# Performance work log

Hardware: AMD Instinct MI355X
Metric: run time of the kernel (lower is better)

Reference implementation:

```python
import jax, jax.numpy as jnp
import numpy as np

NEG_SLOPE = 0.2  # PyG GATConv default negative_slope


def _glorot(key, shape):
    fan = shape[0]
    return jax.random.normal(key, shape, dtype=jnp.float32) / np.sqrt(fan)


def setup_inputs() -> dict:
    key = jax.random.key(0)
    ks = jax.random.split(key, 32)
    N, E, C_IN, C_H, C_OUT = 20000, 320000, 128, 640, 2
    inp = {
        "x": jax.random.normal(ks[0], (N, C_IN), dtype=jnp.float32),
        "edge_index": jax.random.randint(ks[1], (2, E), 0, N, dtype=jnp.int64),
    }
    dims = [(C_IN, C_H), (C_H, C_H), (C_H, C_H), (C_H, C_H), (C_H, C_OUT)]
    for i, (ci, co) in enumerate(dims, start=1):
        k = jax.random.split(ks[1 + i], 4)
        inp[f"W{i}"] = _glorot(k[0], (ci, co))
        inp[f"as{i}"] = _glorot(k[1], (co,))
        inp[f"ad{i}"] = _glorot(k[2], (co,))
        inp[f"b{i}"] = jnp.zeros((co,), dtype=jnp.float32)
    return inp


def _gat_conv(h, W, a_src, a_dst, b, src, dst, N):
    # h: [N, Ci] -> hW: [N, Co]
    hW = h @ W
    # per-edge attention logit: LeakyReLU(alpha_src[j] + alpha_dst[i]) for edge j->i
    e = jax.nn.leaky_relu((hW @ a_src)[src] + (hW @ a_dst)[dst], NEG_SLOPE)
    # segment softmax over incoming edges of each dst node (self-loops guarantee nonempty)
    m = jax.ops.segment_max(e, dst, num_segments=N)
    ex = jnp.exp(e - m[dst])
    den = jax.ops.segment_sum(ex, dst, num_segments=N)
    alpha = ex / den[dst]
    # weighted scatter-add of source messages
    out = jax.ops.segment_sum(alpha[:, None] * hW[src], dst, num_segments=N)
    return out + b


def reference(x, edge_index, W1, as1, ad1, b1, W2, as2, ad2, b2, W3, as3, ad3, b3,
              W4, as4, ad4, b4, W5, as5, ad5, b5):
    N = x.shape[0]
    # PyG GATConv default add_self_loops=True
    loops = jnp.arange(N, dtype=edge_index.dtype)
    ei = jnp.concatenate([edge_index, jnp.stack([loops, loops])], axis=1)
    src, dst = ei[0], ei[1]
    h = jax.nn.relu(_gat_conv(x, W1, as1, ad1, b1, src, dst, N))
    h = jax.nn.relu(_gat_conv(h, W2, as2, ad2, b2, src, dst, N))
    h = jax.nn.relu(_gat_conv(h, W3, as3, ad3, b3, src, dst, N))
    h = jax.nn.relu(_gat_conv(h, W4, as4, ad4, b4, src, dst, N))
    # dropout in eval mode = identity
    return _gat_conv(h, W5, as5, ad5, b5, src, dst, N)
```

## Files before the change

kernel.cpp:

```cpp
#include <hip/hip_runtime.h>
#include <math.h>

#define N_NODES 20000
#define MPAD 20096
#define E_EDGES 320000
#define ET (E_EDGES + N_NODES)
#define C_HID 640
#define NEG_SLOPE 0.2f

typedef __attribute__((ext_vector_type(8))) short bf16x8;
typedef __attribute__((ext_vector_type(4))) float f32x4;

__device__ __forceinline__ float leaky(float x) { return x > 0.f ? x : NEG_SLOPE * x; }

__device__ __forceinline__ unsigned short f2bf(float f) {
    unsigned u = __float_as_uint(f);
    unsigned r = (u + 0x7fffu + ((u >> 16) & 1u)) >> 16;
    return (unsigned short)r;
}
__device__ __forceinline__ float bf2f(unsigned short h) {
    return __uint_as_float(((unsigned)h) << 16);
}

__device__ __forceinline__ void gld16(const void* g, void* l) {
    __builtin_amdgcn_global_load_lds((const __attribute__((address_space(1))) unsigned int*)g,
                                     (__attribute__((address_space(3))) unsigned int*)l,
                                     16, 0, 0);
}

__global__ void k_zero(int* p, int n) {
    int i = blockIdx.x * blockDim.x + threadIdx.x;
    if (i < n) p[i] = 0;
}

__global__ void k_zerof(float* p, int n) {
    int i = blockIdx.x * blockDim.x + threadIdx.x;
    if (i < n) p[i] = 0.f;
}

__global__ void k_count(const int* __restrict__ ei, int* __restrict__ counts) {
    int j = blockIdx.x * blockDim.x + threadIdx.x;
    if (j >= ET) return;
    int d = (j < E_EDGES) ? ei[E_EDGES + j] : (j - E_EDGES);
    atomicAdd(&counts[d], 1);
}

__global__ __launch_bounds__(1024) void k_scan(const int* __restrict__ counts,
                                               int* __restrict__ rowptr) {
    __shared__ int part[1024];
    int t = threadIdx.x;
    int base = t * 20;
    int incl[20];
    int s = 0;
#pragma unroll
    for (int k = 0; k < 20; k++) {
        int i = base + k;
        int v = (i < N_NODES) ? counts[i] : 0;
        s += v;
        incl[k] = s;
    }
    part[t] = s;
    __syncthreads();
    for (int off = 1; off < 1024; off <<= 1) {
        int x = (t >= off) ? part[t - off] : 0;
        __syncthreads();
        part[t] += x;
        __syncthreads();
    }
    int prefix = (t == 0) ? 0 : part[t - 1];
    if (t == 0) rowptr[0] = 0;
#pragma unroll
    for (int k = 0; k < 20; k++) {
        int i = base + k;
        if (i < N_NODES) rowptr[i + 1] = prefix + incl[k];
    }
}

__global__ void k_copy(const int* __restrict__ a, int* __restrict__ b, int n) {
    int i = blockIdx.x * blockDim.x + threadIdx.x;
    if (i < n) b[i] = a[i];
}

__global__ void k_fill(const int* __restrict__ ei, int* __restrict__ cursor, int* __restrict__ col) {
    int j = blockIdx.x * blockDim.x + threadIdx.x;
    if (j >= ET) return;
    int s, d;
    if (j < E_EDGES) { s = ei[j]; d = ei[E_EDGES + j]; }
    else { s = d = j - E_EDGES; }
    int pos = atomicAdd(&cursor[d], 1);
    col[pos] = s;
}

__global__ void k_splitx(const float* __restrict__ x, unsigned short* __restrict__ xh,
                         unsigned short* __restrict__ xl) {
    int idx = blockIdx.x * blockDim.x + threadIdx.x;
    if (idx >= MPAD * 128 / 4) return;
    int row = idx >> 5;
    float4 v = make_float4(0.f, 0.f, 0.f, 0.f);
    if (row < N_NODES) v = ((const float4*)x)[idx];
    float a[4] = {v.x, v.y, v.z, v.w};
    unsigned short h[4], l[4];
#pragma unroll
    for (int i = 0; i < 4; i++) {
        h[i] = f2bf(a[i]);
        l[i] = f2bf(a[i] - bf2f(h[i]));
    }
    *(ushort4*)&xh[idx * 4] = make_ushort4(h[0], h[1], h[2], h[3]);
    *(ushort4*)&xl[idx * 4] = make_ushort4(l[0], l[1], l[2], l[3]);
}

__global__ void k_splitW(const float* __restrict__ W, unsigned short* __restrict__ Wth,
                         unsigned short* __restrict__ Wtl, int K) {
    int idx = blockIdx.x * blockDim.x + threadIdx.x;
    if (idx >= K * C_HID) return;
    int k = idx / C_HID, n = idx - k * C_HID;
    float w = W[idx];
    unsigned short h = f2bf(w);
    Wth[n * K + k] = h;
    Wtl[n * K + k] = f2bf(w - bf2f(h));
}

__global__ void k_padzero(unsigned short* __restrict__ ph, unsigned short* __restrict__ pl) {
    int idx = blockIdx.x * blockDim.x + threadIdx.x;
    int total = (MPAD - N_NODES) * C_HID;
    if (idx >= total) return;
    ph[N_NODES * C_HID + idx] = 0;
    pl[N_NODES * C_HID + idx] = 0;
}

__global__ __launch_bounds__(256) void k_mfma_gemm(
    const unsigned short* __restrict__ Ahi, const unsigned short* __restrict__ Alo,
    const unsigned short* __restrict__ Bth, const unsigned short* __restrict__ Btl,
    float* __restrict__ C, int K, int M,
    const float* __restrict__ asrc, const float* __restrict__ adst,
    float* __restrict__ as_, float* __restrict__ ad_) {
    __shared__ unsigned short lds[4 * 128 * 32];
    const int t = threadIdx.x;
    const int lane = t & 63, wv = t >> 6;
    const int wm = wv & 1, wn = wv >> 1;
    const int quad = lane >> 4, cl = lane & 15;
    const int rowBase = blockIdx.x * 128;
    const int colBase = blockIdx.y * 128;
    const int r = t >> 2, c8 = (t & 3) * 8;

    f32x4 acc[4][4];
#pragma unroll
    for (int i = 0; i < 4; i++)
#pragma unroll
        for (int j = 0; j < 4; j++)
            acc[i][j] = (f32x4){0.f, 0.f, 0.f, 0.f};

    for (int k0 = 0; k0 < K; k0 += 32) {
        __syncthreads();
#pragma unroll
        for (int p = 0; p < 2; ++p) {
            int row = p * 64 + r;
            size_t ga = (size_t)(rowBase + row) * K + k0 + c8;
            size_t gb = (size_t)(colBase + row) * K + k0 + c8;
            int lo = row * 32 + c8;
            gld16(Ahi + ga, &lds[lo]);
            gld16(Alo + ga, &lds[4096 + lo]);
            gld16(Bth + gb, &lds[8192 + lo]);
            gld16(Btl + gb, &lds[12288 + lo]);
        }
        __syncthreads();

        bf16x8 ah[4], al[4], bh[4], bl[4];
#pragma unroll
        for (int i = 0; i < 4; ++i) {
            int am = (wm * 64 + i * 16 + cl) * 32 + quad * 8;
            ah[i] = *(const bf16x8*)&lds[am];
            al[i] = *(const bf16x8*)&lds[4096 + am];
            int bn = (wn * 64 + i * 16 + cl) * 32 + quad * 8;
            bh[i] = *(const bf16x8*)&lds[8192 + bn];
            bl[i] = *(const bf16x8*)&lds[12288 + bn];
        }
#pragma unroll
        for (int i = 0; i < 4; ++i)
#pragma unroll
            for (int j = 0; j < 4; ++j) {
                acc[i][j] = __builtin_amdgcn_mfma_f32_16x16x32_bf16(ah[i], bh[j], acc[i][j], 0, 0, 0);
                acc[i][j] = __builtin_amdgcn_mfma_f32_16x16x32_bf16(ah[i], bl[j], acc[i][j], 0, 0, 0);
                acc[i][j] = __builtin_amdgcn_mfma_f32_16x16x32_bf16(al[i], bh[j], acc[i][j], 0, 0, 0);
            }
    }

#pragma unroll
    for (int i = 0; i < 4; ++i)
#pragma unroll
        for (int j = 0; j < 4; ++j) {
            int colC = colBase + wn * 64 + j * 16 + cl;
#pragma unroll
            for (int rr = 0; rr < 4; ++rr) {
                int rowC = rowBase + wm * 64 + i * 16 + quad * 4 + rr;
                if (rowC < M) C[(size_t)rowC * C_HID + colC] = acc[i][j][rr];
            }
        }

    float av[4], dv[4];
#pragma unroll
    for (int j = 0; j < 4; ++j) {
        int cn = colBase + wn * 64 + j * 16 + cl;
        av[j] = asrc[cn];
        dv[j] = adst[cn];
    }
#pragma unroll
    for (int i = 0; i < 4; ++i)
#pragma unroll
        for (int rr = 0; rr < 4; ++rr) {
            float s = 0.f, d = 0.f;
#pragma unroll
            for (int j = 0; j < 4; ++j) {
                float v = acc[i][j][rr];
                s = fmaf(v, av[j], s);
                d = fmaf(v, dv[j], d);
            }
#pragma unroll
            for (int o = 8; o >= 1; o >>= 1) {
                s += __shfl_xor(s, o);
                d += __shfl_xor(d, o);
            }
            int rowC = rowBase + wm * 64 + i * 16 + quad * 4 + rr;
            if (cl == 0 && rowC < M) {
                atomicAdd(&as_[rowC], s);
                atomicAdd(&ad_[rowC], d);
            }
        }
}

__global__ __launch_bounds__(256) void k_gather(const float* __restrict__ hW,
                                                const float* __restrict__ as_,
                                                const float* __restrict__ ad_,
                                                const int* __restrict__ rowptr,
                                                const int* __restrict__ col,
                                                const float* __restrict__ bias,
                                                unsigned short* __restrict__ outh,
                                                unsigned short* __restrict__ outl) {
    int wv = threadIdx.x >> 6, lane = threadIdx.x & 63;
    int node = blockIdx.x * 4 + wv;
    int c = blockIdx.y;
    if (node >= N_NODES) return;
    int start = rowptr[node], end = rowptr[node + 1];
    int deg = end - start;
    const float* base = hW + c * 128 + lane * 2;
    float ax = 0.f, ay = 0.f;
    float adi = ad_[node];

    if (deg <= 64) {
        int col_v = col[start + min(lane, deg - 1)];
        float asv = as_[col_v];
        float logit = (lane < deg) ? leaky(asv + adi) : -1e30f;
        float m = logit;
#pragma unroll
        for (int o = 32; o; o >>= 1) m = fmaxf(m, __shfl_xor(m, o));
        float ex = __expf(logit - m);
        float den = ex;
#pragma unroll
        for (int o = 32; o; o >>= 1) den += __shfl_xor(den, o);
        float alpha_v = ex / den;

        for (int e0 = 0; e0 < deg; e0 += 8) {
            float2 r[8];
            float a[8];
#pragma unroll
            for (int q = 0; q < 8; ++q) {
                int e = e0 + q;
                int ec = min(e, deg - 1);
                int s = __shfl(col_v, ec);
                float ar = __shfl(alpha_v, ec);
                a[q] = (e < deg) ? ar : 0.f;
                r[q] = *(const float2*)(base + (size_t)s * C_HID);
            }
#pragma unroll
            for (int q = 0; q < 8; ++q) {
                ax = fmaf(a[q], r[q].x, ax);
                ay = fmaf(a[q], r[q].y, ay);
            }
        }
    } else {
        float m = -1e30f;
        for (int j = start + lane; j < end; j += 64)
            m = fmaxf(m, leaky(as_[col[j]] + adi));
        for (int o = 32; o; o >>= 1) m = fmaxf(m, __shfl_xor(m, o));
        float den = 0.f;
        for (int j = start + lane; j < end; j += 64)
            den += __expf(leaky(as_[col[j]] + adi) - m);
        for (int o = 32; o; o >>= 1) den += __shfl_xor(den, o);
        float inv = 1.f / den;
        for (int j = start; j < end; ++j) {
            int s = col[j];
            float a = __expf(leaky(as_[s] + adi) - m) * inv;
            float2 r = *(const float2*)(base + (size_t)s * C_HID);
            ax = fmaf(a, r.x, ax);
            ay = fmaf(a, r.y, ay);
        }
    }

    float2 b = *(const float2*)&bias[c * 128 + lane * 2];
    float v0 = fmaxf(ax + b.x, 0.f);
    float v1 = fmaxf(ay + b.y, 0.f);
    unsigned short h0 = f2bf(v0), h1 = f2bf(v1);
    size_t o = (size_t)node * C_HID + c * 128 + lane * 2;
    *(ushort2*)&outh[o] = make_ushort2(h0, h1);
    *(ushort2*)&outl[o] = make_ushort2(f2bf(v0 - bf2f(h0)), f2bf(v1 - bf2f(h1)));
}

__global__ __launch_bounds__(256) void k_gemm2(const unsigned short* __restrict__ hh,
                                               const unsigned short* __restrict__ hl,
                                               const float* __restrict__ W,
                                               const float* __restrict__ asrc,
                                               const float* __restrict__ adst,
                                               float* __restrict__ hW5,
                                               float* __restrict__ as_,
                                               float* __restrict__ ad_) {
    int wave = (blockIdx.x * blockDim.x + threadIdx.x) >> 6;
    int lane = threadIdx.x & 63;
    if (wave >= N_NODES) return;
    const ushort2* rh = (const ushort2*)(hh + (size_t)wave * C_HID);
    const ushort2* rl = (const ushort2*)(hl + (size_t)wave * C_HID);
    float a0 = 0.f, a1 = 0.f;
#pragma unroll
    for (int k2 = lane; k2 < C_HID / 2; k2 += 64) {
        ushort2 h2 = rh[k2];
        ushort2 l2 = rl[k2];
        float v0 = bf2f(h2.x) + bf2f(l2.x);
        float v1 = bf2f(h2.y) + bf2f(l2.y);
        int k = k2 * 2;
        a0 = fmaf(v0, W[k * 2 + 0], a0);
        a1 = fmaf(v0, W[k * 2 + 1], a1);
        a0 = fmaf(v1, W[k * 2 + 2], a0);
        a1 = fmaf(v1, W[k * 2 + 3], a1);
    }
    for (int o = 32; o; o >>= 1) { a0 += __shfl_xor(a0, o); a1 += __shfl_xor(a1, o); }
    if (lane == 0) {
        hW5[wave * 2 + 0] = a0;
        hW5[wave * 2 + 1] = a1;
        as_[wave] = a0 * asrc[0] + a1 * asrc[1];
        ad_[wave] = a0 * adst[0] + a1 * adst[1];
    }
}

__global__ __launch_bounds__(256) void k_agg2(const float* __restrict__ hW5,
                                              const float* __restrict__ as_,
                                              const float* __restrict__ ad_,
                                              const int* __restrict__ rowptr,
                                              const int* __restrict__ col,
                                              const float* __restrict__ bias,
                                              float* __restrict__ out) {
    int wv = threadIdx.x >> 6, lane = threadIdx.x & 63;
    int node = blockIdx.x * 4 + wv;
    if (node >= N_NODES) return;
    int start = rowptr[node], end = rowptr[node + 1];
    int deg = end - start;
    float adi = ad_[node];
    float o0, o1;
    if (deg <= 64) {
        int cv = col[start + min(lane, deg - 1)];
        float logit = (lane < deg) ? leaky(as_[cv] + adi) : -1e30f;
        float m = logit;
#pragma unroll
        for (int o = 32; o; o >>= 1) m = fmaxf(m, __shfl_xor(m, o));
        float ex = __expf(logit - m);
        float den = ex;
#pragma unroll
        for (int o = 32; o; o >>= 1) den += __shfl_xor(den, o);
        float al = ex / den;
        float2 hv = make_float2(0.f, 0.f);
        if (lane < deg) hv = *(const float2*)&hW5[cv * 2];
        o0 = al * hv.x; o1 = al * hv.y;
#pragma unroll
        for (int o = 32; o; o >>= 1) { o0 += __shfl_xor(o0, o); o1 += __shfl_xor(o1, o); }
    } else {
        float m = -1e30f;
        for (int j = start + lane; j < end; j += 64)
            m = fmaxf(m, leaky(as_[col[j]] + adi));
        for (int o = 32; o; o >>= 1) m = fmaxf(m, __shfl_xor(m, o));
        float den = 0.f;
        for (int j = start + lane; j < end; j += 64)
            den += __expf(leaky(as_[col[j]] + adi) - m);
        for (int o = 32; o; o >>= 1) den += __shfl_xor(den, o);
        float inv = 1.f / den;
        o0 = 0.f; o1 = 0.f;
        for (int j = start + lane; j < end; j += 64) {
            int s = col[j];
            float al = __expf(leaky(as_[s] + adi) - m) * inv;
            o0 = fmaf(al, hW5[s * 2 + 0], o0);
            o1 = fmaf(al, hW5[s * 2 + 1], o1);
        }
        for (int o = 32; o; o >>= 1) { o0 += __shfl_xor(o0, o); o1 += __shfl_xor(o1, o); }
    }
    if (lane == 0) {
        out[node * 2 + 0] = o0 + bias[0];
        out[node * 2 + 1] = o1 + bias[1];
    }
}

extern "C" void kernel_launch(void* const* d_in, const int* in_sizes, int n_in,
                              void* d_out, int out_size, void* d_ws, size_t ws_size,
                              hipStream_t stream) {
    const float* x   = (const float*)d_in[0];
    const int*   ei  = (const int*)d_in[1];
    const float* W[5]  = {(const float*)d_in[2],  (const float*)d_in[6],
                          (const float*)d_in[10], (const float*)d_in[14],
                          (const float*)d_in[18]};
    const float* As[5] = {(const float*)d_in[3],  (const float*)d_in[7],
                          (const float*)d_in[11], (const float*)d_in[15],
                          (const float*)d_in[19]};
    const float* Ad[5] = {(const float*)d_in[4],  (const float*)d_in[8],
                          (const float*)d_in[12], (const float*)d_in[16],
                          (const float*)d_in[20]};
    const float* Bi[5] = {(const float*)d_in[5],  (const float*)d_in[9],
                          (const float*)d_in[13], (const float*)d_in[17],
                          (const float*)d_in[21]};
    float* out = (float*)d_out;

    char* w = (char*)d_ws;
    float* bufX = (float*)w;                 w += (size_t)N_NODES * C_HID * 4;
    unsigned short* pair_hi = (unsigned short*)w; w += (size_t)MPAD * C_HID * 2;
    unsigned short* pair_lo = (unsigned short*)w; w += (size_t)MPAD * C_HID * 2;
    unsigned short* Wth = (unsigned short*)w;     w += (size_t)C_HID * C_HID * 2;
    unsigned short* Wtl = (unsigned short*)w;     w += (size_t)C_HID * C_HID * 2;
    float* as_  = (float*)w;  w += N_NODES * 4;
    float* ad_  = (float*)w;  w += N_NODES * 4;
    float* hW5  = (float*)w;  w += N_NODES * 2 * 4;
    int* rowptr = (int*)w;    w += (N_NODES + 1) * 4 + 12;
    int* counts = (int*)w;    w += N_NODES * 4;
    int* col    = (int*)w;    w += ET * 4;

    const int TB = 256;
    k_zero<<<(N_NODES + TB - 1) / TB, TB, 0, stream>>>(counts, N_NODES);
    k_count<<<(ET + TB - 1) / TB, TB, 0, stream>>>(ei, counts);
    k_scan<<<1, 1024, 0, stream>>>(counts, rowptr);
    k_copy<<<(N_NODES + TB - 1) / TB, TB, 0, stream>>>(rowptr, counts, N_NODES);
    k_fill<<<(ET + TB - 1) / TB, TB, 0, stream>>>(ei, counts, col);

    k_padzero<<<((MPAD - N_NODES) * C_HID + TB - 1) / TB, TB, 0, stream>>>(pair_hi, pair_lo);
    k_splitx<<<(MPAD * 128 / 4 + TB - 1) / TB, TB, 0, stream>>>(x, pair_hi, pair_lo);

    dim3 gemmGrid(MPAD / 128, C_HID / 128);
    dim3 gathGrid(N_NODES / 4, 5);
    int nodeWaveBlocks = (N_NODES + 3) / 4;

    for (int l = 0; l <= 3; ++l) {
        int K = (l == 0) ? 128 : C_HID;
        k_zerof<<<(2 * N_NODES + TB - 1) / TB, TB, 0, stream>>>(as_, 2 * N_NODES);
        k_splitW<<<(K * C_HID + TB - 1) / TB, TB, 0, stream>>>(W[l], Wth, Wtl, K);
        k_mfma_gemm<<<gemmGrid, TB, 0, stream>>>(pair_hi, pair_lo, Wth, Wtl, bufX, K, N_NODES,
                                                 As[l], Ad[l], as_, ad_);
        k_gather<<<gathGrid, TB, 0, stream>>>(bufX, as_, ad_, rowptr, col, Bi[l], pair_hi, pair_lo);
    }

    k_gemm2<<<nodeWaveBlocks, TB, 0, stream>>>(pair_hi, pair_lo, W[4], As[4], Ad[4], hW5, as_, ad_);
    k_agg2<<<nodeWaveBlocks, TB, 0, stream>>>(hW5, as_, ad_, rowptr, col, Bi[4], out);
}
```

Baseline: 855.3 us.

## Reorder layer-1 GAT as aggregate-then-transform on 128-wide input

```diff
diff --git a/kernel.cpp b/kernel.cpp
--- a/kernel.cpp
+++ b/kernel.cpp
@@ -6,6 +6,7 @@
 #define E_EDGES 320000
 #define ET (E_EDGES + N_NODES)
 #define C_HID 640
+#define C_IN 128
 #define NEG_SLOPE 0.2f
 
 typedef __attribute__((ext_vector_type(8))) short bf16x8;
@@ -45,7 +46,7 @@
     atomicAdd(&counts[d], 1);
 }
 
-__global__ __launch_bounds__(1024) void k_scan(const int* __restrict__ counts,
+__global__ __launch_bounds__(1024) void k_scan(int* __restrict__ counts,
                                                int* __restrict__ rowptr) {
     __shared__ int part[1024];
     int t = threadIdx.x;
@@ -72,13 +73,11 @@
 #pragma unroll
     for (int k = 0; k < 20; k++) {
         int i = base + k;
-        if (i < N_NODES) rowptr[i + 1] = prefix + incl[k];
-    }
-}
-
-__global__ void k_copy(const int* __restrict__ a, int* __restrict__ b, int n) {
-    int i = blockIdx.x * blockDim.x + threadIdx.x;
-    if (i < n) b[i] = a[i];
+        if (i < N_NODES) {
+            rowptr[i + 1] = prefix + incl[k];
+            counts[i] = (k == 0) ? prefix : prefix + incl[k - 1];
+        }
+    }
 }
 
 __global__ void k_fill(const int* __restrict__ ei, int* __restrict__ cursor, int* __restrict__ col) {
@@ -89,24 +88,6 @@
     else { s = d = j - E_EDGES; }
     int pos = atomicAdd(&cursor[d], 1);
     col[pos] = s;
-}
-
-__global__ void k_splitx(const float* __restrict__ x, unsigned short* __restrict__ xh,
-                         unsigned short* __restrict__ xl) {
-    int idx = blockIdx.x * blockDim.x + threadIdx.x;
-    if (idx >= MPAD * 128 / 4) return;
-    int row = idx >> 5;
-    float4 v = make_float4(0.f, 0.f, 0.f, 0.f);
-    if (row < N_NODES) v = ((const float4*)x)[idx];
-    float a[4] = {v.x, v.y, v.z, v.w};
-    unsigned short h[4], l[4];
-#pragma unroll
-    for (int i = 0; i < 4; i++) {
-        h[i] = f2bf(a[i]);
-        l[i] = f2bf(a[i] - bf2f(h[i]));
-    }
-    *(ushort4*)&xh[idx * 4] = make_ushort4(h[0], h[1], h[2], h[3]);
-    *(ushort4*)&xl[idx * 4] = make_ushort4(l[0], l[1], l[2], l[3]);
 }
 
 __global__ void k_splitW(const float* __restrict__ W, unsigned short* __restrict__ Wth,
@@ -120,12 +101,53 @@
     Wtl[n * K + k] = f2bf(w - bf2f(h));
 }
 
-__global__ void k_padzero(unsigned short* __restrict__ ph, unsigned short* __restrict__ pl) {
+__global__ void k_padzero(unsigned short* __restrict__ xah, unsigned short* __restrict__ xal,
+                          unsigned short* __restrict__ ph, unsigned short* __restrict__ pl) {
     int idx = blockIdx.x * blockDim.x + threadIdx.x;
-    int total = (MPAD - N_NODES) * C_HID;
-    if (idx >= total) return;
-    ph[N_NODES * C_HID + idx] = 0;
-    pl[N_NODES * C_HID + idx] = 0;
+    const int nx = (MPAD - N_NODES) * C_IN;
+    const int np = (MPAD - N_NODES) * C_HID;
+    if (idx < nx) {
+        xah[N_NODES * C_IN + idx] = 0;
+        xal[N_NODES * C_IN + idx] = 0;
+    }
+    if (idx < np) {
+        ph[N_NODES * C_HID + idx] = 0;
+        pl[N_NODES * C_HID + idx] = 0;
+    }
+}
+
+__global__ void k_wa(const float* __restrict__ W, const float* __restrict__ a_s,
+                     const float* __restrict__ a_d,
+                     float* __restrict__ ws_, float* __restrict__ wd_) {
+    int wave = (blockIdx.x * blockDim.x + threadIdx.x) >> 6;
+    int lane = threadIdx.x & 63;
+    if (wave >= C_IN) return;
+    const float* row = W + (size_t)wave * C_HID;
+    float s = 0.f, d = 0.f;
+#pragma unroll
+    for (int c = lane; c < C_HID; c += 64) {
+        float w = row[c];
+        s = fmaf(w, a_s[c], s);
+        d = fmaf(w, a_d[c], d);
+    }
+    for (int o = 32; o; o >>= 1) { s += __shfl_xor(s, o); d += __shfl_xor(d, o); }
+    if (lane == 0) { ws_[wave] = s; wd_[wave] = d; }
+}
+
+__global__ __launch_bounds__(256) void k_logitx(const float* __restrict__ x,
+                                                const float* __restrict__ ws_,
+                                                const float* __restrict__ wd_,
+                                                float* __restrict__ as_, float* __restrict__ ad_) {
+    int wave = (blockIdx.x * blockDim.x + threadIdx.x) >> 6;
+    int lane = threadIdx.x & 63;
+    if (wave >= N_NODES) return;
+    float2 xv = ((const float2*)(x + (size_t)wave * C_IN))[lane];
+    float2 wsv = ((const float2*)ws_)[lane];
+    float2 wdv = ((const float2*)wd_)[lane];
+    float s = xv.x * wsv.x + xv.y * wsv.y;
+    float d = xv.x * wdv.x + xv.y * wdv.y;
+    for (int o = 32; o; o >>= 1) { s += __shfl_xor(s, o); d += __shfl_xor(d, o); }
+    if (lane == 0) { as_[wave] = s; ad_[wave] = d; }
 }
 
 __global__ __launch_bounds__(256) void k_mfma_gemm(
@@ -226,6 +248,81 @@
                 atomicAdd(&ad_[rowC], d);
             }
         }
+}
+
+__global__ __launch_bounds__(256) void k_mfma_gemm_pair(
+    const unsigned short* __restrict__ Ahi, const unsigned short* __restrict__ Alo,
+    const unsigned short* __restrict__ Bth, const unsigned short* __restrict__ Btl,
+    unsigned short* __restrict__ Oh, unsigned short* __restrict__ Ol,
+    const float* __restrict__ bias, int K, int M) {
+    __shared__ unsigned short lds[4 * 128 * 32];
+    const int t = threadIdx.x;
+    const int lane = t & 63, wv = t >> 6;
+    const int wm = wv & 1, wn = wv >> 1;
+    const int quad = lane >> 4, cl = lane & 15;
+    const int rowBase = blockIdx.x * 128;
+    const int colBase = blockIdx.y * 128;
+    const int r = t >> 2, c8 = (t & 3) * 8;
+
+    f32x4 acc[4][4];
+#pragma unroll
+    for (int i = 0; i < 4; i++)
+#pragma unroll
+        for (int j = 0; j < 4; j++)
+            acc[i][j] = (f32x4){0.f, 0.f, 0.f, 0.f};
+
+    for (int k0 = 0; k0 < K; k0 += 32) {
+        __syncthreads();
+#pragma unroll
+        for (int p = 0; p < 2; ++p) {
+            int row = p * 64 + r;
+            size_t ga = (size_t)(rowBase + row) * K + k0 + c8;
+            size_t gb = (size_t)(colBase + row) * K + k0 + c8;
+            int lo = row * 32 + c8;
+            gld16(Ahi + ga, &lds[lo]);
+            gld16(Alo + ga, &lds[4096 + lo]);
+            gld16(Bth + gb, &lds[8192 + lo]);
+            gld16(Btl + gb, &lds[12288 + lo]);
+        }
+        __syncthreads();
+
+        bf16x8 ah[4], al[4], bh[4], bl[4];
+#pragma unroll
+        for (int i = 0; i < 4; ++i) {
+            int am = (wm * 64 + i * 16 + cl) * 32 + quad * 8;
+            ah[i] = *(const bf16x8*)&lds[am];
+            al[i] = *(const bf16x8*)&lds[4096 + am];
+            int bn = (wn * 64 + i * 16 + cl) * 32 + quad * 8;
+            bh[i] = *(const bf16x8*)&lds[8192 + bn];
+            bl[i] = *(const bf16x8*)&lds[12288 + bn];
+        }
+#pragma unroll
+        for (int i = 0; i < 4; ++i)
+#pragma unroll
+            for (int j = 0; j < 4; ++j) {
+                acc[i][j] = __builtin_amdgcn_mfma_f32_16x16x32_bf16(ah[i], bh[j], acc[i][j], 0, 0, 0);
+                acc[i][j] = __builtin_amdgcn_mfma_f32_16x16x32_bf16(ah[i], bl[j], acc[i][j], 0, 0, 0);
+                acc[i][j] = __builtin_amdgcn_mfma_f32_16x16x32_bf16(al[i], bh[j], acc[i][j], 0, 0, 0);
+            }
+    }
+
+#pragma unroll
+    for (int j = 0; j < 4; ++j) {
+        int colC = colBase + wn * 64 + j * 16 + cl;
+        float bv = bias[colC];
+#pragma unroll
+        for (int i = 0; i < 4; ++i)
+#pragma unroll
+            for (int rr = 0; rr < 4; ++rr) {
+                int rowC = rowBase + wm * 64 + i * 16 + quad * 4 + rr;
+                if (rowC < M) {
+                    float v = fmaxf(acc[i][j][rr] + bv, 0.f);
+                    unsigned short h = f2bf(v);
+                    Oh[(size_t)rowC * C_HID + colC] = h;
+                    Ol[(size_t)rowC * C_HID + colC] = f2bf(v - bf2f(h));
+                }
+            }
+    }
 }
 
 __global__ __launch_bounds__(256) void k_gather(const float* __restrict__ hW,
@@ -303,6 +400,78 @@
     size_t o = (size_t)node * C_HID + c * 128 + lane * 2;
     *(ushort2*)&outh[o] = make_ushort2(h0, h1);
     *(ushort2*)&outl[o] = make_ushort2(f2bf(v0 - bf2f(h0)), f2bf(v1 - bf2f(h1)));
+}
+
+__global__ __launch_bounds__(256) void k_gather_x(const float* __restrict__ x,
+                                                  const float* __restrict__ as_,
+                                                  const float* __restrict__ ad_,
+                                                  const int* __restrict__ rowptr,
+                                                  const int* __restrict__ col,
+                                                  unsigned short* __restrict__ outh,
+                                                  unsigned short* __restrict__ outl) {
+    int wv = threadIdx.x >> 6, lane = threadIdx.x & 63;
+    int node = blockIdx.x * 4 + wv;
+    if (node >= N_NODES) return;
+    int start = rowptr[node], end = rowptr[node + 1];
+    int deg = end - start;
+    const float* base = x + lane * 2;
+    float ax = 0.f, ay = 0.f;
+    float adi = ad_[node];
+
+    if (deg <= 64) {
+        int col_v = col[start + min(lane, deg - 1)];
+        float asv = as_[col_v];
+        float logit = (lane < deg) ? leaky(asv + adi) : -1e30f;
+        float m = logit;
+#pragma unroll
+        for (int o = 32; o; o >>= 1) m = fmaxf(m, __shfl_xor(m, o));
+        float ex = __expf(logit - m);
+        float den = ex;
+#pragma unroll
+        for (int o = 32; o; o >>= 1) den += __shfl_xor(den, o);
+        float alpha_v = ex / den;
+
+        for (int e0 = 0; e0 < deg; e0 += 8) {
+            float2 r[8];
+            float a[8];
+#pragma unroll
+            for (int q = 0; q < 8; ++q) {
+                int e = e0 + q;
+                int ec = min(e, deg - 1);
+                int s = __shfl(col_v, ec);
+                float ar = __shfl(alpha_v, ec);
+                a[q] = (e < deg) ? ar : 0.f;
+                r[q] = *(const float2*)(base + (size_t)s * C_IN);
+            }
+#pragma unroll
+            for (int q = 0; q < 8; ++q) {
+                ax = fmaf(a[q], r[q].x, ax);
+                ay = fmaf(a[q], r[q].y, ay);
+            }
+        }
+    } else {
+        float m = -1e30f;
+        for (int j = start + lane; j < end; j += 64)
+            m = fmaxf(m, leaky(as_[col[j]] + adi));
+        for (int o = 32; o; o >>= 1) m = fmaxf(m, __shfl_xor(m, o));
+        float den = 0.f;
+        for (int j = start + lane; j < end; j += 64)
+            den += __expf(leaky(as_[col[j]] + adi) - m);
+        for (int o = 32; o; o >>= 1) den += __shfl_xor(den, o);
+        float inv = 1.f / den;
+        for (int j = start; j < end; ++j) {
+            int s = col[j];
+            float a = __expf(leaky(as_[s] + adi) - m) * inv;
+            float2 r = *(const float2*)(base + (size_t)s * C_IN);
+            ax = fmaf(a, r.x, ax);
+            ay = fmaf(a, r.y, ay);
+        }
+    }
+
+    unsigned short h0 = f2bf(ax), h1 = f2bf(ay);
+    size_t o = (size_t)node * C_IN + lane * 2;
+    *(ushort2*)&outh[o] = make_ushort2(h0, h1);
+    *(ushort2*)&outl[o] = make_ushort2(f2bf(ax - bf2f(h0)), f2bf(ay - bf2f(h1)));
 }
 
 __global__ __launch_bounds__(256) void k_gemm2(const unsigned short* __restrict__ hh,
@@ -416,6 +585,8 @@
 
     char* w = (char*)d_ws;
     float* bufX = (float*)w;                 w += (size_t)N_NODES * C_HID * 4;
+    unsigned short* xa_hi = (unsigned short*)bufX;
+    unsigned short* xa_lo = xa_hi + (size_t)MPAD * C_IN;
     unsigned short* pair_hi = (unsigned short*)w; w += (size_t)MPAD * C_HID * 2;
     unsigned short* pair_lo = (unsigned short*)w; w += (size_t)MPAD * C_HID * 2;
     unsigned short* Wth = (unsigned short*)w;     w += (size_t)C_HID * C_HID * 2;
@@ -423,6 +594,8 @@
     float* as_  = (float*)w;  w += N_NODES * 4;
     float* ad_  = (float*)w;  w += N_NODES * 4;
     float* hW5  = (float*)w;  w += N_NODES * 2 * 4;
+    float* ws_  = (float*)w;  w += C_IN * 4;
+    float* wd_  = (float*)w;  w += C_IN * 4;
     int* rowptr = (int*)w;    w += (N_NODES + 1) * 4 + 12;
     int* counts = (int*)w;    w += N_NODES * 4;
     int* col    = (int*)w;    w += ET * 4;
@@ -431,21 +604,25 @@
     k_zero<<<(N_NODES + TB - 1) / TB, TB, 0, stream>>>(counts, N_NODES);
     k_count<<<(ET + TB - 1) / TB, TB, 0, stream>>>(ei, counts);
     k_scan<<<1, 1024, 0, stream>>>(counts, rowptr);
-    k_copy<<<(N_NODES + TB - 1) / TB, TB, 0, stream>>>(rowptr, counts, N_NODES);
     k_fill<<<(ET + TB - 1) / TB, TB, 0, stream>>>(ei, counts, col);
 
-    k_padzero<<<((MPAD - N_NODES) * C_HID + TB - 1) / TB, TB, 0, stream>>>(pair_hi, pair_lo);
-    k_splitx<<<(MPAD * 128 / 4 + TB - 1) / TB, TB, 0, stream>>>(x, pair_hi, pair_lo);
+    k_padzero<<<((MPAD - N_NODES) * C_HID + TB - 1) / TB, TB, 0, stream>>>(xa_hi, xa_lo, pair_hi, pair_lo);
 
     dim3 gemmGrid(MPAD / 128, C_HID / 128);
     dim3 gathGrid(N_NODES / 4, 5);
     int nodeWaveBlocks = (N_NODES + 3) / 4;
 
-    for (int l = 0; l <= 3; ++l) {
-        int K = (l == 0) ? 128 : C_HID;
+    k_splitW<<<(C_IN * C_HID + TB - 1) / TB, TB, 0, stream>>>(W[0], Wth, Wtl, C_IN);
+    k_wa<<<32, TB, 0, stream>>>(W[0], As[0], Ad[0], ws_, wd_);
+    k_logitx<<<nodeWaveBlocks, TB, 0, stream>>>(x, ws_, wd_, as_, ad_);
+    k_gather_x<<<nodeWaveBlocks, TB, 0, stream>>>(x, as_, ad_, rowptr, col, xa_hi, xa_lo);
+    k_mfma_gemm_pair<<<gemmGrid, TB, 0, stream>>>(xa_hi, xa_lo, Wth, Wtl,
+                                                  pair_hi, pair_lo, Bi[0], C_IN, N_NODES);
+
+    for (int l = 1; l <= 3; ++l) {
         k_zerof<<<(2 * N_NODES + TB - 1) / TB, TB, 0, stream>>>(as_, 2 * N_NODES);
-        k_splitW<<<(K * C_HID + TB - 1) / TB, TB, 0, stream>>>(W[l], Wth, Wtl, K);
-        k_mfma_gemm<<<gemmGrid, TB, 0, stream>>>(pair_hi, pair_lo, Wth, Wtl, bufX, K, N_NODES,
+        k_splitW<<<(C_HID * C_HID + TB - 1) / TB, TB, 0, stream>>>(W[l], Wth, Wtl, C_HID);
+        k_mfma_gemm<<<gemmGrid, TB, 0, stream>>>(pair_hi, pair_lo, Wth, Wtl, bufX, C_HID, N_NODES,
                                                  As[l], Ad[l], as_, ad_);
         k_gather<<<gathGrid, TB, 0, stream>>>(bufX, as_, ad_, rowptr, col, Bi[l], pair_hi, pair_lo);
     }
```

New measurement: 814.9 us. 1.05x faster.
